# Performance work log

Hardware: AMD Instinct MI355X
Metric: run time of the kernel (lower is better)

Reference implementation:

```python
import jax, jax.numpy as jnp
import numpy as np

MODEL_DIM = 128
N_FRAMES = 128
N_SAMPLES = 2 ** 15
N_TABLES = 16
TABLE_SIZE = 512
STD = 0.01


def _mlp(x, w1, b1, w2, b2, w3, b3):
    h = jax.nn.leaky_relu(x @ w1 + b1, 0.2)
    h = jax.nn.leaky_relu(h @ w2 + b2, 0.2)
    return h @ w3 + b3


def _interp_linear(x, out_size):
    # x: (B, T_in) -> (B, out_size); torch F.interpolate(mode='linear', align_corners=False)
    t_in = x.shape[-1]
    pos = (jnp.arange(out_size, dtype=x.dtype) + 0.5) * (t_in / out_size) - 0.5
    pos = jnp.clip(pos, 0.0, t_in - 1.0)
    lo = jnp.floor(pos).astype(jnp.int32)
    hi = jnp.minimum(lo + 1, t_in - 1)
    w = pos - lo.astype(x.dtype)
    return x[:, lo] * (1.0 - w) + x[:, hi] * w


def setup_inputs() -> dict:
    key = jax.random.key(0)
    ks = jax.random.split(key, 11)

    def lin(k, i, o):
        kw, kb = jax.random.split(k)
        return (jax.random.normal(kw, (i, o), jnp.float32) * (0.1 / np.sqrt(i)),
                jax.random.normal(kb, (o,), jnp.float32) * 0.01)

    x = jax.random.normal(ks[0], (8, MODEL_DIM), jnp.float32)
    wavetables = jax.random.uniform(ks[1], (N_TABLES, TABLE_SIZE), jnp.float32, -1.0, 1.0)
    tc_w1, tc_b1 = lin(ks[2], MODEL_DIM, MODEL_DIM)
    tc_w2, tc_b2 = lin(ks[3], MODEL_DIM, MODEL_DIM)
    tc_w3, tc_b3 = lin(ks[4], MODEL_DIM, N_TABLES * 16)
    env_w1, env_b1 = lin(ks[5], MODEL_DIM, MODEL_DIM)
    env_w2, env_b2 = lin(ks[6], MODEL_DIM, MODEL_DIM)
    env_w3, env_b3 = lin(ks[7], MODEL_DIM, N_FRAMES)
    fr_w1, fr_b1 = lin(ks[8], MODEL_DIM, MODEL_DIM)
    fr_w2, fr_b2 = lin(ks[9], MODEL_DIM, MODEL_DIM)
    fr_w3, fr_b3 = lin(ks[10], MODEL_DIM, N_FRAMES)
    return dict(x=x, wavetables=wavetables,
                tc_w1=tc_w1, tc_b1=tc_b1, tc_w2=tc_w2, tc_b2=tc_b2, tc_w3=tc_w3, tc_b3=tc_b3,
                env_w1=env_w1, env_b1=env_b1, env_w2=env_w2, env_b2=env_b2, env_w3=env_w3, env_b3=env_b3,
                fr_w1=fr_w1, fr_b1=fr_b1, fr_w2=fr_w2, fr_b2=fr_b2, fr_w3=fr_w3, fr_b3=fr_b3)


def reference(x, wavetables,
              tc_w1, tc_b1, tc_w2, tc_b2, tc_w3, tc_b3,
              env_w1, env_b1, env_w2, env_b2, env_w3, env_b3,
              fr_w1, fr_b1, fr_w2, fr_b2, fr_w3, fr_b3):
    batch = x.shape[0]

    # table choice head -> per-item table selection (reconstructs `indices`/`values` in source)
    tc = _mlp(x, tc_w1, tc_b1, tc_w2, tc_b2, tc_w3, tc_b3).reshape(batch, N_TABLES, 16)
    scores = tc.mean(axis=-1)                       # (B, n_tables)
    indices = jnp.argmax(scores, axis=-1)           # (B,)
    values = jnp.max(scores, axis=-1)               # (B,)

    # normalized wavetables
    wt = wavetables / (jnp.max(wavetables, axis=-1, keepdims=True) + 1e-8)
    selected_tables = wt[indices][:, None, :]       # (B, 1, table_size)

    # amplitude envelope
    env = _mlp(x, env_w1, env_b1, env_w2, env_b2, env_w3, env_b3)  # (B, n_frames)
    env = _interp_linear(env ** 2, N_SAMPLES)       # (B, n_samples)

    # instantaneous frequency -> phase in [0, 1)
    freq = _mlp(x, fr_w1, fr_b1, fr_w2, fr_b2, fr_w3, fr_b3) ** 2  # (B, n_frames)
    freq = _interp_linear(freq, N_SAMPLES)          # (B, n_samples)
    phase = jnp.cumsum(freq, axis=-1) % 1.0         # (B, n_samples)

    # Gaussian pdf sampling kernel over table positions: (B, table_size, n_samples)
    grid = jnp.linspace(0.0, 1.0, TABLE_SIZE)
    z = (grid[None, :, None] - phase[:, None, :]) / STD
    kernel = jnp.exp(-0.5 * z * z) / (STD * np.sqrt(2.0 * np.pi))
    sampling_kernel = jnp.transpose(kernel, (0, 2, 1))  # (B, n_samples, table_size)

    # resample the selected table via batched matmul
    sampled = selected_tables @ kernel              # (B, 1, n_samples)
    sampled = sampled * env[:, None, :] * values[:, None, None]
    return sampled, sampling_kernel
```

## Files before the change

kernel.cpp:

```cpp
#include <hip/hip_runtime.h>
#include <hip/hip_bf16.h>
#include <math.h>

typedef __hip_bfloat16 bf16;

#define BATCH    8
#define DIM      128
#define NFRAMES  128
#define NSAMP    32768
#define NTAB     16
#define TSIZE    512

__device__ __forceinline__ float ld(const void* p, int i, bool f32) {
    return f32 ? ((const float*)p)[i] : __bfloat162float(((const bf16*)p)[i]);
}

#define WS_VALUES 0
#define WS_ENV    64
#define WS_FREQ   1088
#define WS_SEL    2112
#define WS_PHASE  6208

__global__ __launch_bounds__(256) void k1_mlp(
    const void* __restrict__ x, const void* __restrict__ wav,
    const void* tw1, const void* tb1, const void* tw2, const void* tb2,
    const void* tw3, const void* tb3,
    const void* ew1, const void* eb1, const void* ew2, const void* eb2,
    const void* ew3, const void* eb3,
    const void* fw1, const void* fb1, const void* fw2, const void* fb2,
    const void* fw3, const void* fb3,
    float* __restrict__ ws)
{
    const int head = blockIdx.x;
    const int tid  = threadIdx.x;

    __shared__ int s_isf32;
    __shared__ float xs[BATCH*DIM];
    __shared__ float h1[BATCH*DIM];
    __shared__ float h2[BATCH*DIM];
    __shared__ float o3[BATCH*256];
    __shared__ float scores[BATCH*16];
    __shared__ int   idxs[BATCH];
    __shared__ float red[256];

    if (tid == 0) s_isf32 = 0;
    __syncthreads();
    {
        const unsigned short* xb = (const unsigned short*)x;
        bool big = false;
        for (int i = tid; i < BATCH*DIM; i += 256) {
            const int e = (xb[i] >> 7) & 0xFF;
            if (e >= 132) big = true;
        }
        if (big) s_isf32 = 1;
    }
    __syncthreads();
    const bool F32 = (s_isf32 != 0);

    const void *W1, *B1, *W2, *B2, *W3, *B3;
    int od3;
    if (head == 0)      { W1=tw1; B1=tb1; W2=tw2; B2=tb2; W3=tw3; B3=tb3; od3=256; }
    else if (head == 1) { W1=ew1; B1=eb1; W2=ew2; B2=eb2; W3=ew3; B3=eb3; od3=128; }
    else                { W1=fw1; B1=fb1; W2=fw2; B2=fb2; W3=fw3; B3=fb3; od3=128; }

    for (int i = tid; i < BATCH*DIM; i += 256) xs[i] = ld(x, i, F32);
    __syncthreads();

    {
        const int o = tid & 127, bs = tid >> 7;
        double acc[4];
        const double bb = (double)ld(B1, o, F32);
        #pragma unroll
        for (int j = 0; j < 4; j++) acc[j] = bb;
        for (int k = 0; k < DIM; k++) {
            const float wv = ld(W1, k*DIM + o, F32);
            #pragma unroll
            for (int j = 0; j < 4; j++)
                acc[j] += (double)xs[(bs + 2*j)*DIM + k] * (double)wv;
        }
        #pragma unroll
        for (int j = 0; j < 4; j++) {
            float v = (float)acc[j];
            v = v > 0.f ? v : 0.2f*v;
            h1[(bs + 2*j)*DIM + o] = v;
        }
    }
    __syncthreads();

    {
        const int o = tid & 127, bs = tid >> 7;
        double acc[4];
        const double bb = (double)ld(B2, o, F32);
        #pragma unroll
        for (int j = 0; j < 4; j++) acc[j] = bb;
        for (int k = 0; k < DIM; k++) {
            const float wv = ld(W2, k*DIM + o, F32);
            #pragma unroll
            for (int j = 0; j < 4; j++)
                acc[j] += (double)h1[(bs + 2*j)*DIM + k] * (double)wv;
        }
        #pragma unroll
        for (int j = 0; j < 4; j++) {
            float v = (float)acc[j];
            v = v > 0.f ? v : 0.2f*v;
            h2[(bs + 2*j)*DIM + o] = v;
        }
    }
    __syncthreads();

    if (od3 == 256) {
        const int o = tid;
        double acc[8];
        const double bb = (double)ld(B3, o, F32);
        #pragma unroll
        for (int b = 0; b < 8; b++) acc[b] = bb;
        for (int k = 0; k < DIM; k++) {
            const float wv = ld(W3, k*256 + o, F32);
            #pragma unroll
            for (int b = 0; b < 8; b++)
                acc[b] += (double)h2[b*DIM + k] * (double)wv;
        }
        #pragma unroll
        for (int b = 0; b < 8; b++) o3[b*256 + o] = (float)acc[b];
    } else {
        const int o = tid & 127, bs = tid >> 7;
        double acc[4];
        const double bb = (double)ld(B3, o, F32);
        #pragma unroll
        for (int j = 0; j < 4; j++) acc[j] = bb;
        for (int k = 0; k < DIM; k++) {
            const float wv = ld(W3, k*DIM + o, F32);
            #pragma unroll
            for (int j = 0; j < 4; j++)
                acc[j] += (double)h2[(bs + 2*j)*DIM + k] * (double)wv;
        }
        #pragma unroll
        for (int j = 0; j < 4; j++) o3[(bs + 2*j)*DIM + o] = (float)acc[j];
    }
    __syncthreads();

    if (head == 0) {
        if (tid < 128) {
            const int b = tid >> 4, i = tid & 15;
            float s = 0.f;
            for (int j = 0; j < 16; j++) s += o3[b*256 + i*16 + j];
            scores[b*16 + i] = s * (1.0f/16.0f);
        }
        __syncthreads();
        if (tid < 8) {
            const int b = tid;
            float best = scores[b*16]; int bi = 0;
            for (int i = 1; i < 16; i++) {
                const float v = scores[b*16 + i];
                if (v > best) { best = v; bi = i; }
            }
            idxs[b] = bi;
            ws[WS_VALUES + b] = best;
        }
        __syncthreads();
        for (int b = 0; b < 8; b++) {
            const int idx = idxs[b];
            float m = -1e30f;
            for (int t = tid; t < TSIZE; t += 256)
                m = fmaxf(m, ld(wav, idx*TSIZE + t, F32));
            red[tid] = m;
            __syncthreads();
            for (int off = 128; off; off >>= 1) {
                if (tid < off) red[tid] = fmaxf(red[tid], red[tid + off]);
                __syncthreads();
            }
            const float mx = red[0] + 1e-8f;
            for (int t = tid; t < TSIZE; t += 256)
                ws[WS_SEL + b*TSIZE + t] = ld(wav, idx*TSIZE + t, F32) / mx;
            __syncthreads();
        }
    } else {
        float* dst = ws + (head == 1 ? WS_ENV : WS_FREQ);
        for (int i = tid; i < BATCH*NFRAMES; i += 256) {
            const float v = o3[i];
            dst[i] = v * v;
        }
    }
}

__global__ __launch_bounds__(1024) void k2_phase(float* __restrict__ ws)
{
    const int b = blockIdx.x;
    const int t = threadIdx.x;
    __shared__ float  fr[NFRAMES];
    __shared__ double sums[1024];

    if (t < NFRAMES) fr[t] = ws[WS_FREQ + b*NFRAMES + t];
    __syncthreads();

    const int SPT = NSAMP / 1024;
    const int s0  = t * SPT;
    double v[32];
    double local = 0.0;
    #pragma unroll
    for (int i = 0; i < SPT; i++) {
        const int s = s0 + i;
        double pos = ((double)s + 0.5) * (1.0/256.0) - 0.5;
        pos = fmin(fmax(pos, 0.0), 127.0);
        const int lo = (int)pos;
        int hi = lo + 1; if (hi > 127) hi = 127;
        const double w = pos - (double)lo;
        const double f = (double)fr[lo] * (1.0 - w) + (double)fr[hi] * w;
        v[i] = f;
        local += f;
    }
    sums[t] = local;
    __syncthreads();

    for (int off = 1; off < 1024; off <<= 1) {
        const double add = (t >= off) ? sums[t - off] : 0.0;
        __syncthreads();
        sums[t] += add;
        __syncthreads();
    }

    double run = sums[t] - local;
    float* phase = ws + WS_PHASE + (size_t)b * NSAMP;
    #pragma unroll
    for (int i = 0; i < SPT; i++) {
        run += v[i];
        phase[s0 + i] = (float)(run - floor(run));
    }
}

__global__ __launch_bounds__(256) void k3_synth(const float* __restrict__ ws,
                                                float* __restrict__ out)
{
    const int lane = threadIdx.x & 63;
    const int row  = (blockIdx.x << 2) + (threadIdx.x >> 6);
    const int b    = row >> 15;
    const int s    = row & (NSAMP - 1);

    const float p = ws[WS_PHASE + row];

    float pos = ((float)s + 0.5f) * (1.0f/256.0f) - 0.5f;
    pos = fminf(fmaxf(pos, 0.0f), 127.0f);
    const int lo = (int)pos;
    int hi = lo + 1; if (hi > 127) hi = 127;
    const float w = pos - (float)lo;
    const float* envf = ws + WS_ENV + b*NFRAMES;
    const float env = envf[lo]*(1.0f - w) + envf[hi]*w;
    const float val = ws[WS_VALUES + b];

    float* krow = out + (size_t)BATCH*NSAMP + ((size_t)row << 9);
    const float* tab = ws + WS_SEL + b*TSIZE;

    float dot = 0.f;
    #pragma unroll
    for (int j = 0; j < 2; j++) {
        const int t0 = 4*lane + 256*j;
        const float4 tv = *reinterpret_cast<const float4*>(tab + t0);
        const float tb4[4] = {tv.x, tv.y, tv.z, tv.w};
        float pv[4];
        #pragma unroll
        for (int k = 0; k < 4; k++) {
            const float g = (float)(t0 + k) * (1.0f/511.0f);
            const float z = (g - p) * 100.0f;
            const float e = __expf(-0.5f*z*z) * 39.89422804014327f;
            dot += e * tb4[k];
            pv[k] = e;
        }
        float4 o4; o4.x = pv[0]; o4.y = pv[1]; o4.z = pv[2]; o4.w = pv[3];
        *reinterpret_cast<float4*>(krow + t0) = o4;
    }

    #pragma unroll
    for (int m = 32; m; m >>= 1) dot += __shfl_xor(dot, m, 64);
    if (lane == 0)
        out[row] = dot * env * val;
}

extern "C" void kernel_launch(void* const* d_in, const int* in_sizes, int n_in,
                              void* d_out, int out_size, void* d_ws, size_t ws_size,
                              hipStream_t stream)
{
    float* ws  = (float*)d_ws;
    float* out = (float*)d_out;

    hipLaunchKernelGGL(k1_mlp, dim3(3), dim3(256), 0, stream,
        d_in[0], d_in[1],
        d_in[2],  d_in[3],  d_in[4],  d_in[5],  d_in[6],  d_in[7],
        d_in[8],  d_in[9],  d_in[10], d_in[11], d_in[12], d_in[13],
        d_in[14], d_in[15], d_in[16], d_in[17], d_in[18], d_in[19],
        ws);

    hipLaunchKernelGGL(k2_phase, dim3(BATCH), dim3(1024), 0, stream, ws);

    hipLaunchKernelGGL(k3_synth, dim3((BATCH*NSAMP)/4), dim3(256), 0, stream,
        ws, out);
}
```

Baseline: 656.5 us.

## Fuse MLP heads with phase scan per batch and coarsen synth rows

Merges the three-block MLP kernel and the phase-scan kernel into one per-batch kernel that runs all three heads, table normalisation and the cumulative sum, which removes a launch and spreads the MLP across 8 blocks instead of 3. The synth kernel now handles four rows per wavefront. It hoists the table loads, writes the large sampling-kernel output with nontemporal stores, and stores the four samples as one vector. The output write of about 512MB dominates, so the gain likely depends mostly on how well the stores stream.

```diff
diff --git a/kernel.cpp b/kernel.cpp
--- a/kernel.cpp
+++ b/kernel.cpp
@@ -3,6 +3,7 @@
 #include <math.h>
 
 typedef __hip_bfloat16 bf16;
+typedef float f32x4 __attribute__((ext_vector_type(4)));
 
 #define BATCH    8
 #define DIM      128
@@ -21,7 +22,7 @@
 #define WS_SEL    2112
 #define WS_PHASE  6208
 
-__global__ __launch_bounds__(256) void k1_mlp(
+__global__ __launch_bounds__(1024) void kA_prep(
     const void* __restrict__ x, const void* __restrict__ wav,
     const void* tw1, const void* tb1, const void* tw2, const void* tb2,
     const void* tw3, const void* tb3,
@@ -31,170 +32,119 @@
     const void* fw3, const void* fb3,
     float* __restrict__ ws)
 {
-    const int head = blockIdx.x;
-    const int tid  = threadIdx.x;
-
-    __shared__ int s_isf32;
-    __shared__ float xs[BATCH*DIM];
-    __shared__ float h1[BATCH*DIM];
-    __shared__ float h2[BATCH*DIM];
-    __shared__ float o3[BATCH*256];
-    __shared__ float scores[BATCH*16];
-    __shared__ int   idxs[BATCH];
-    __shared__ float red[256];
+    const int b   = blockIdx.x;
+    const int tid = threadIdx.x;
+
+    __shared__ int    s_isf32;
+    __shared__ float  xs[DIM];
+    __shared__ float  h1s[3][DIM];
+    __shared__ float  h2s[3][DIM];
+    __shared__ float  o3tc[256];
+    __shared__ float  envf[NFRAMES];
+    __shared__ float  frf[NFRAMES];
+    __shared__ float  scores[16];
+    __shared__ float  red[512];
+    __shared__ int    s_idx;
+    __shared__ double sums[1024];
 
     if (tid == 0) s_isf32 = 0;
     __syncthreads();
     {
         const unsigned short* xb = (const unsigned short*)x;
-        bool big = false;
-        for (int i = tid; i < BATCH*DIM; i += 256) {
-            const int e = (xb[i] >> 7) & 0xFF;
-            if (e >= 132) big = true;
+        if (tid < 1024) {
+            const int e = (xb[tid] >> 7) & 0xFF;
+            if (e >= 132) s_isf32 = 1;
         }
-        if (big) s_isf32 = 1;
     }
     __syncthreads();
     const bool F32 = (s_isf32 != 0);
 
-    const void *W1, *B1, *W2, *B2, *W3, *B3;
-    int od3;
-    if (head == 0)      { W1=tw1; B1=tb1; W2=tw2; B2=tb2; W3=tw3; B3=tb3; od3=256; }
-    else if (head == 1) { W1=ew1; B1=eb1; W2=ew2; B2=eb2; W3=ew3; B3=eb3; od3=128; }
-    else                { W1=fw1; B1=fb1; W2=fw2; B2=fb2; W3=fw3; B3=fb3; od3=128; }
-
-    for (int i = tid; i < BATCH*DIM; i += 256) xs[i] = ld(x, i, F32);
-    __syncthreads();
-
-    {
-        const int o = tid & 127, bs = tid >> 7;
-        double acc[4];
-        const double bb = (double)ld(B1, o, F32);
-        #pragma unroll
-        for (int j = 0; j < 4; j++) acc[j] = bb;
-        for (int k = 0; k < DIM; k++) {
-            const float wv = ld(W1, k*DIM + o, F32);
-            #pragma unroll
-            for (int j = 0; j < 4; j++)
-                acc[j] += (double)xs[(bs + 2*j)*DIM + k] * (double)wv;
-        }
-        #pragma unroll
-        for (int j = 0; j < 4; j++) {
-            float v = (float)acc[j];
-            v = v > 0.f ? v : 0.2f*v;
-            h1[(bs + 2*j)*DIM + o] = v;
-        }
-    }
-    __syncthreads();
-
-    {
-        const int o = tid & 127, bs = tid >> 7;
-        double acc[4];
-        const double bb = (double)ld(B2, o, F32);
-        #pragma unroll
-        for (int j = 0; j < 4; j++) acc[j] = bb;
-        for (int k = 0; k < DIM; k++) {
-            const float wv = ld(W2, k*DIM + o, F32);
-            #pragma unroll
-            for (int j = 0; j < 4; j++)
-                acc[j] += (double)h1[(bs + 2*j)*DIM + k] * (double)wv;
-        }
-        #pragma unroll
-        for (int j = 0; j < 4; j++) {
-            float v = (float)acc[j];
-            v = v > 0.f ? v : 0.2f*v;
-            h2[(bs + 2*j)*DIM + o] = v;
-        }
-    }
-    __syncthreads();
-
-    if (od3 == 256) {
+    if (tid < DIM) xs[tid] = ld(x, b*DIM + tid, F32);
+    __syncthreads();
+
+    const void* W1h[3] = {tw1, ew1, fw1};
+    const void* B1h[3] = {tb1, eb1, fb1};
+    const void* W2h[3] = {tw2, ew2, fw2};
+    const void* B2h[3] = {tb2, eb2, fb2};
+
+    if (tid < 384) {
+        const int head = tid >> 7, o = tid & 127;
+        double acc = (double)ld(B1h[head], o, F32);
+        const void* W = W1h[head];
+        for (int k = 0; k < DIM; k++)
+            acc += (double)xs[k] * (double)ld(W, k*DIM + o, F32);
+        float v = (float)acc;
+        h1s[head][o] = v > 0.f ? v : 0.2f*v;
+    }
+    __syncthreads();
+
+    if (tid < 384) {
+        const int head = tid >> 7, o = tid & 127;
+        double acc = (double)ld(B2h[head], o, F32);
+        const void* W = W2h[head];
+        const float* hh = h1s[head];
+        for (int k = 0; k < DIM; k++)
+            acc += (double)hh[k] * (double)ld(W, k*DIM + o, F32);
+        float v = (float)acc;
+        h2s[head][o] = v > 0.f ? v : 0.2f*v;
+    }
+    __syncthreads();
+
+    if (tid < 256) {
         const int o = tid;
-        double acc[8];
-        const double bb = (double)ld(B3, o, F32);
-        #pragma unroll
-        for (int b = 0; b < 8; b++) acc[b] = bb;
-        for (int k = 0; k < DIM; k++) {
-            const float wv = ld(W3, k*256 + o, F32);
-            #pragma unroll
-            for (int b = 0; b < 8; b++)
-                acc[b] += (double)h2[b*DIM + k] * (double)wv;
-        }
-        #pragma unroll
-        for (int b = 0; b < 8; b++) o3[b*256 + o] = (float)acc[b];
-    } else {
-        const int o = tid & 127, bs = tid >> 7;
-        double acc[4];
-        const double bb = (double)ld(B3, o, F32);
-        #pragma unroll
-        for (int j = 0; j < 4; j++) acc[j] = bb;
-        for (int k = 0; k < DIM; k++) {
-            const float wv = ld(W3, k*DIM + o, F32);
-            #pragma unroll
-            for (int j = 0; j < 4; j++)
-                acc[j] += (double)h2[(bs + 2*j)*DIM + k] * (double)wv;
-        }
-        #pragma unroll
-        for (int j = 0; j < 4; j++) o3[(bs + 2*j)*DIM + o] = (float)acc[j];
-    }
-    __syncthreads();
-
-    if (head == 0) {
-        if (tid < 128) {
-            const int b = tid >> 4, i = tid & 15;
-            float s = 0.f;
-            for (int j = 0; j < 16; j++) s += o3[b*256 + i*16 + j];
-            scores[b*16 + i] = s * (1.0f/16.0f);
-        }
+        double acc = (double)ld(tb3, o, F32);
+        const float* hh = h2s[0];
+        for (int k = 0; k < DIM; k++)
+            acc += (double)hh[k] * (double)ld(tw3, k*256 + o, F32);
+        o3tc[o] = (float)acc;
+    } else if (tid < 384) {
+        const int o = tid - 256;
+        double acc = (double)ld(eb3, o, F32);
+        const float* hh = h2s[1];
+        for (int k = 0; k < DIM; k++)
+            acc += (double)hh[k] * (double)ld(ew3, k*DIM + o, F32);
+        const float v = (float)acc;
+        envf[o] = v * v;
+    } else if (tid < 512) {
+        const int o = tid - 384;
+        double acc = (double)ld(fb3, o, F32);
+        const float* hh = h2s[2];
+        for (int k = 0; k < DIM; k++)
+            acc += (double)hh[k] * (double)ld(fw3, k*DIM + o, F32);
+        const float v = (float)acc;
+        frf[o] = v * v;
+    }
+    __syncthreads();
+
+    if (tid < 16) {
+        float s = 0.f;
+        for (int j = 0; j < 16; j++) s += o3tc[tid*16 + j];
+        scores[tid] = s * (1.0f/16.0f);
+    }
+    __syncthreads();
+    if (tid == 0) {
+        float best = scores[0]; int bi = 0;
+        for (int i = 1; i < 16; i++)
+            if (scores[i] > best) { best = scores[i]; bi = i; }
+        s_idx = bi;
+        ws[WS_VALUES + b] = best;
+    }
+    __syncthreads();
+
+    const int idx = s_idx;
+    float wv_t = 0.f;
+    if (tid < 512) { wv_t = ld(wav, idx*TSIZE + tid, F32); red[tid] = wv_t; }
+    __syncthreads();
+    for (int off = 256; off; off >>= 1) {
+        if (tid < off) red[tid] = fmaxf(red[tid], red[tid + off]);
         __syncthreads();
-        if (tid < 8) {
-            const int b = tid;
-            float best = scores[b*16]; int bi = 0;
-            for (int i = 1; i < 16; i++) {
-                const float v = scores[b*16 + i];
-                if (v > best) { best = v; bi = i; }
-            }
-            idxs[b] = bi;
-            ws[WS_VALUES + b] = best;
-        }
-        __syncthreads();
-        for (int b = 0; b < 8; b++) {
-            const int idx = idxs[b];
-            float m = -1e30f;
-            for (int t = tid; t < TSIZE; t += 256)
-                m = fmaxf(m, ld(wav, idx*TSIZE + t, F32));
-            red[tid] = m;
-            __syncthreads();
-            for (int off = 128; off; off >>= 1) {
-                if (tid < off) red[tid] = fmaxf(red[tid], red[tid + off]);
-                __syncthreads();
-            }
-            const float mx = red[0] + 1e-8f;
-            for (int t = tid; t < TSIZE; t += 256)
-                ws[WS_SEL + b*TSIZE + t] = ld(wav, idx*TSIZE + t, F32) / mx;
-            __syncthreads();
-        }
-    } else {
-        float* dst = ws + (head == 1 ? WS_ENV : WS_FREQ);
-        for (int i = tid; i < BATCH*NFRAMES; i += 256) {
-            const float v = o3[i];
-            dst[i] = v * v;
-        }
-    }
-}
-
-__global__ __launch_bounds__(1024) void k2_phase(float* __restrict__ ws)
-{
-    const int b = blockIdx.x;
-    const int t = threadIdx.x;
-    __shared__ float  fr[NFRAMES];
-    __shared__ double sums[1024];
-
-    if (t < NFRAMES) fr[t] = ws[WS_FREQ + b*NFRAMES + t];
-    __syncthreads();
+    }
+    const float mx = red[0] + 1e-8f;
+    if (tid < 512) ws[WS_SEL + b*TSIZE + tid] = wv_t / mx;
+    if (tid < NFRAMES) ws[WS_ENV + b*NFRAMES + tid] = envf[tid];
 
     const int SPT = NSAMP / 1024;
-    const int s0  = t * SPT;
+    const int s0  = tid * SPT;
     double v[32];
     double local = 0.0;
     #pragma unroll
@@ -205,21 +155,19 @@
         const int lo = (int)pos;
         int hi = lo + 1; if (hi > 127) hi = 127;
         const double w = pos - (double)lo;
-        const double f = (double)fr[lo] * (1.0 - w) + (double)fr[hi] * w;
+        const double f = (double)frf[lo] * (1.0 - w) + (double)frf[hi] * w;
         v[i] = f;
         local += f;
     }
-    sums[t] = local;
-    __syncthreads();
-
+    sums[tid] = local;
+    __syncthreads();
     for (int off = 1; off < 1024; off <<= 1) {
-        const double add = (t >= off) ? sums[t - off] : 0.0;
+        const double add = (tid >= off) ? sums[tid - off] : 0.0;
         __syncthreads();
-        sums[t] += add;
+        sums[tid] += add;
         __syncthreads();
     }
-
-    double run = sums[t] - local;
+    double run = sums[tid] - local;
     float* phase = ws + WS_PHASE + (size_t)b * NSAMP;
     #pragma unroll
     for (int i = 0; i < SPT; i++) {
@@ -228,51 +176,62 @@
     }
 }
 
-__global__ __launch_bounds__(256) void k3_synth(const float* __restrict__ ws,
+__global__ __launch_bounds__(256) void kB_synth(const float* __restrict__ ws,
                                                 float* __restrict__ out)
 {
     const int lane = threadIdx.x & 63;
-    const int row  = (blockIdx.x << 2) + (threadIdx.x >> 6);
-    const int b    = row >> 15;
-    const int s    = row & (NSAMP - 1);
-
-    const float p = ws[WS_PHASE + row];
-
-    float pos = ((float)s + 0.5f) * (1.0f/256.0f) - 0.5f;
-    pos = fminf(fmaxf(pos, 0.0f), 127.0f);
-    const int lo = (int)pos;
-    int hi = lo + 1; if (hi > 127) hi = 127;
-    const float w = pos - (float)lo;
+    const int w    = (blockIdx.x << 2) + (threadIdx.x >> 6);
+    const int r0   = w << 2;
+    const int b    = r0 >> 15;
+
+    const float* tab = ws + WS_SEL + b*TSIZE;
+    const f32x4 tv0 = *reinterpret_cast<const f32x4*>(tab + 4*lane);
+    const f32x4 tv1 = *reinterpret_cast<const f32x4*>(tab + 4*lane + 256);
+    const float  val  = ws[WS_VALUES + b];
     const float* envf = ws + WS_ENV + b*NFRAMES;
-    const float env = envf[lo]*(1.0f - w) + envf[hi]*w;
-    const float val = ws[WS_VALUES + b];
-
-    float* krow = out + (size_t)BATCH*NSAMP + ((size_t)row << 9);
-    const float* tab = ws + WS_SEL + b*TSIZE;
-
-    float dot = 0.f;
+    float* kbase = out + (size_t)BATCH*NSAMP + ((size_t)r0 << 9);
+
+    float samp[4];
     #pragma unroll
-    for (int j = 0; j < 2; j++) {
-        const int t0 = 4*lane + 256*j;
-        const float4 tv = *reinterpret_cast<const float4*>(tab + t0);
-        const float tb4[4] = {tv.x, tv.y, tv.z, tv.w};
-        float pv[4];
+    for (int i = 0; i < 4; i++) {
+        const int r = r0 + i;
+        const int s = r & (NSAMP - 1);
+        const float p = ws[WS_PHASE + r];
+
+        float pos = ((float)s + 0.5f) * (1.0f/256.0f) - 0.5f;
+        pos = fminf(fmaxf(pos, 0.0f), 127.0f);
+        const int lo = (int)pos;
+        int hi = lo + 1; if (hi > 127) hi = 127;
+        const float wq = pos - (float)lo;
+        const float env = envf[lo]*(1.0f - wq) + envf[hi]*wq;
+
+        float dot = 0.f;
         #pragma unroll
-        for (int k = 0; k < 4; k++) {
-            const float g = (float)(t0 + k) * (1.0f/511.0f);
-            const float z = (g - p) * 100.0f;
-            const float e = __expf(-0.5f*z*z) * 39.89422804014327f;
-            dot += e * tb4[k];
-            pv[k] = e;
+        for (int j = 0; j < 2; j++) {
+            const int t0 = 4*lane + 256*j;
+            const f32x4 tv = j ? tv1 : tv0;
+            f32x4 o4;
+            #pragma unroll
+            for (int k = 0; k < 4; k++) {
+                const float g = (float)(t0 + k) * (1.0f/511.0f);
+                const float z = (g - p) * 100.0f;
+                const float e = __expf(-0.5f*z*z) * 39.89422804014327f;
+                dot += e * tv[k];
+                o4[k] = e;
+            }
+            __builtin_nontemporal_store(o4,
+                reinterpret_cast<f32x4*>(kbase + (i << 9) + t0));
         }
-        float4 o4; o4.x = pv[0]; o4.y = pv[1]; o4.z = pv[2]; o4.w = pv[3];
-        *reinterpret_cast<float4*>(krow + t0) = o4;
-    }
-
-    #pragma unroll
-    for (int m = 32; m; m >>= 1) dot += __shfl_xor(dot, m, 64);
-    if (lane == 0)
-        out[row] = dot * env * val;
+
+        #pragma unroll
+        for (int m = 32; m; m >>= 1) dot += __shfl_xor(dot, m, 64);
+        samp[i] = dot * env * val;
+    }
+
+    if (lane == 0) {
+        f32x4 s4; s4[0] = samp[0]; s4[1] = samp[1]; s4[2] = samp[2]; s4[3] = samp[3];
+        *reinterpret_cast<f32x4*>(out + r0) = s4;
+    }
 }
 
 extern "C" void kernel_launch(void* const* d_in, const int* in_sizes, int n_in,
@@ -282,15 +241,13 @@
     float* ws  = (float*)d_ws;
     float* out = (float*)d_out;
 
-    hipLaunchKernelGGL(k1_mlp, dim3(3), dim3(256), 0, stream,
+    hipLaunchKernelGGL(kA_prep, dim3(BATCH), dim3(1024), 0, stream,
         d_in[0], d_in[1],
         d_in[2],  d_in[3],  d_in[4],  d_in[5],  d_in[6],  d_in[7],
         d_in[8],  d_in[9],  d_in[10], d_in[11], d_in[12], d_in[13],
         d_in[14], d_in[15], d_in[16], d_in[17], d_in[18], d_in[19],
         ws);
 
-    hipLaunchKernelGGL(k2_phase, dim3(BATCH), dim3(1024), 0, stream, ws);
-
-    hipLaunchKernelGGL(k3_synth, dim3((BATCH*NSAMP)/4), dim3(256), 0, stream,
+    hipLaunchKernelGGL(kB_synth, dim3((BATCH*NSAMP)/16), dim3(256), 0, stream,
         ws, out);
 }
```

Result: faster. 627.5 us (-4.4%).
